# Kernel optimization log

Measured on AMD Instinct MI355X. Metric: run time of the kernel, lower is better.

## Reference

```python
import jax, jax.numpy as jnp
import numpy as np

B, M, N, K = 8192, 512, 2048, 16
P = 50      # top-k support size per iteration
EPS = 0.01


def soft_threshold(x, theta, p):
    # x: [B, N]
    if p == 0:
        return jnp.sign(x) * jax.nn.relu(jnp.abs(x) - theta)
    abs_ = jnp.abs(x)
    topk_vals, _ = jax.lax.top_k(abs_, p)          # sorted descending
    thresh = topk_vals[:, -1]                      # min of top-k, per row
    keep = (abs_ > thresh[:, None]).astype(x.dtype)
    shrunk = jnp.sign(x) * jax.nn.relu(abs_ - theta)
    return keep * x + (1.0 - keep) * shrunk


def setup_inputs() -> dict:
    key = jax.random.key(0)
    k_y, k_A = jax.random.split(key)
    y = jax.random.normal(k_y, (B, M), dtype=jnp.float32)
    A = jax.random.normal(k_A, (M, N), dtype=jnp.float32) / np.sqrt(M)
    gamma = jnp.full((K,), 3.0, dtype=jnp.float32)
    theta = jnp.full((K,), 0.02, dtype=jnp.float32)
    a_param = jnp.full((K,), 0.01, dtype=jnp.float32)
    v = jnp.ones((K,), dtype=jnp.float32)
    vu = jnp.full((K,), 0.05, dtype=jnp.float32)
    theta_init = jnp.float32(1.0)
    return {"y": y, "A": A, "gamma": gamma, "theta": theta,
            "a_param": a_param, "v": v, "vu": vu,
            "theta_init": theta_init, "info": 0}


def reference(y, A, gamma, theta, a_param, v, vu, theta_init, info):
    # forward_op(x)  = x @ A.T   : [B,N] -> [B,M]
    # backward_op(b) = b @ A     : [B,M] -> [B,N]
    x = jnp.zeros((y.shape[0], A.shape[1]), dtype=y.dtype)
    for i in range(K):
        t = theta_init if i == 0 else theta[i]
        gain = 1.0 + t * vu[i] * jnp.exp(-v[i] * jnp.abs(x))
        b = (gain * x) @ A.T - y                 # residual in measurement space
        c = b @ A                                # gradient step direction
        x_new = soft_threshold(x - gamma[i] * c, theta[i], P)
        overshoot = 1.0 + a_param[i] / (jnp.abs(x_new - x) + EPS)
        x = overshoot * x_new + (1.0 - overshoot) * x
    return (x, jnp.zeros((K, 1), dtype=y.dtype), jnp.zeros((K, 1), dtype=y.dtype))
```

## Files before the change

### kernel.cpp

```cpp
#include <hip/hip_runtime.h>
#include <math.h>

#define Bsz  8192
#define Mdim 512
#define Ndim 2048
#define Kit  16
#define Pk   50
#define EPSv 0.01f

typedef __attribute__((ext_vector_type(8))) short bf16x8;
typedef __attribute__((ext_vector_type(4))) float f32x4;

static __device__ __forceinline__ unsigned short f2bf(float f) {
    unsigned u = __float_as_uint(f);
    return (unsigned short)((u + 0x7fffu + ((u >> 16) & 1u)) >> 16);
}
static __device__ __forceinline__ float bf2f(unsigned short h) {
    return __uint_as_float(((unsigned)h) << 16);
}

static __device__ __forceinline__ void gl16(const void* g, void* l) {
    __builtin_amdgcn_global_load_lds(
        (const __attribute__((address_space(1))) unsigned int*)g,
        (__attribute__((address_space(3))) unsigned int*)l, 16, 0, 0);
}

#define PIPE_BARRIER() __builtin_amdgcn_s_barrier()

#define MFMA3(acc_, bh_, bl_, ah_, al_)                                         \
    acc_ = __builtin_amdgcn_mfma_f32_16x16x32_bf16(bh_, ah_, acc_, 0, 0, 0);    \
    acc_ = __builtin_amdgcn_mfma_f32_16x16x32_bf16(bh_, al_, acc_, 0, 0, 0);    \
    acc_ = __builtin_amdgcn_mfma_f32_16x16x32_bf16(bl_, ah_, acc_, 0, 0, 0);

__global__ __launch_bounds__(256) void presplit_A(
    const float* __restrict__ A, unsigned short* __restrict__ Ah,
    unsigned short* __restrict__ Al, unsigned short* __restrict__ AhT,
    unsigned short* __restrict__ AlT)
{
    int idx = blockIdx.x * 256 + threadIdx.x;
    int m = idx >> 11, n = idx & (Ndim - 1);
    float a = A[idx];
    unsigned short h = f2bf(a);
    unsigned short l = f2bf(a - bf2f(h));
    Ah[idx] = h; Al[idx] = l;
    AhT[(size_t)n * Mdim + m] = h;
    AlT[(size_t)n * Mdim + m] = l;
}

__global__ __launch_bounds__(256) void split_negy_kernel(const float* __restrict__ y,
                                                         unsigned short* __restrict__ bS) {
    int i = blockIdx.x * 256 + threadIdx.x;
    float4 v = ((const float4*)y)[i];
    int idx = i * 4;
    int r = idx >> 9, c = idx & 511;
    float f0 = -v.x, f1 = -v.y, f2 = -v.z, f3 = -v.w;
    unsigned short h0 = f2bf(f0), h1 = f2bf(f1), h2 = f2bf(f2), h3 = f2bf(f3);
    ushort4 hv = make_ushort4(h0, h1, h2, h3);
    ushort4 lv = make_ushort4(f2bf(f0 - bf2f(h0)), f2bf(f1 - bf2f(h1)),
                              f2bf(f2 - bf2f(h2)), f2bf(f3 - bf2f(h3)));
    *(ushort4*)(bS + (size_t)r * 1024 + c)       = hv;
    *(ushort4*)(bS + (size_t)r * 1024 + 512 + c) = lv;
}

__global__ __launch_bounds__(256) void gemm1_mfma(
    const unsigned short* __restrict__ zS,
    const unsigned short* __restrict__ Ah, const unsigned short* __restrict__ Al,
    const float* __restrict__ y, unsigned short* __restrict__ bS)
{
    const int tid  = threadIdx.x;
    const int lane = tid & 63, w = tid >> 6;
    const int lm   = lane & 15, quad = lane >> 4;
    const int wr   = (w & 1) * 64, wm = (w >> 1) * 32;

    int d   = blockIdx.y * gridDim.x + blockIdx.x;
    int sid = (d & 7) * 64 + (d >> 3);
    const int m0 = (sid & 7) * 64, r0 = (sid >> 3) * 128;

    __shared__ __attribute__((aligned(16))) unsigned short zh_s[128 * 64];
    __shared__ __attribute__((aligned(16))) unsigned short zl_s[128 * 64];
    __shared__ __attribute__((aligned(16))) unsigned short ah_s[64 * 64];
    __shared__ __attribute__((aligned(16))) unsigned short al_s[64 * 64];

    f32x4 acc[4][2];
#pragma unroll
    for (int i = 0; i < 4; i++)
#pragma unroll
        for (int j = 0; j < 2; j++) acc[i][j] = (f32x4)0.f;

    const unsigned short* zsh[4]; const unsigned short* zsl[4]; int zoff[4];
#pragma unroll
    for (int s = 0; s < 4; s++) {
        int off = ((w * 4 + s) << 10) + lane * 16;
        int row = off >> 7;
        int kb  = (off & 127) ^ ((row & 7) << 4);
        zoff[s] = (w * 4 + s) << 10;
        zsh[s]  = zS + (size_t)(r0 + row) * 4096 + (kb >> 1);
        zsl[s]  = zS + (size_t)(r0 + row) * 4096 + 2048 + (kb >> 1);
    }
    const unsigned short* ash[2]; const unsigned short* asl[2]; int aoff[2];
#pragma unroll
    for (int s = 0; s < 2; s++) {
        int off = ((w * 2 + s) << 10) + lane * 16;
        int row = off >> 7;
        int kb  = (off & 127) ^ ((row & 7) << 4);
        aoff[s] = (w * 2 + s) << 10;
        ash[s]  = Ah + (size_t)(m0 + row) * 2048 + (kb >> 1);
        asl[s]  = Al + (size_t)(m0 + row) * 2048 + (kb >> 1);
    }

    const int X = (lm & 7) << 4;

    for (int k0 = 0; k0 < Ndim; k0 += 64) {
        __syncthreads();
#pragma unroll
        for (int s = 0; s < 4; s++) {
            gl16(zsh[s], (char*)zh_s + zoff[s]);
            gl16(zsl[s], (char*)zl_s + zoff[s]);
            zsh[s] += 64; zsl[s] += 64;
        }
#pragma unroll
        for (int s = 0; s < 2; s++) {
            gl16(ash[s], (char*)ah_s + aoff[s]);
            gl16(asl[s], (char*)al_s + aoff[s]);
            ash[s] += 64; asl[s] += 64;
        }
        __syncthreads();
#pragma unroll
        for (int kk = 0; kk < 2; kk++) {
            const int cbx = (kk * 64 + quad * 16) ^ X;
            bf16x8 bhf[2], blf[2];
#pragma unroll
            for (int fj = 0; fj < 2; fj++) {
                int ar = wm + fj * 16 + lm;
                bhf[fj] = *(const bf16x8*)((const char*)ah_s + ar * 128 + cbx);
                blf[fj] = *(const bf16x8*)((const char*)al_s + ar * 128 + cbx);
            }
#pragma unroll
            for (int fi = 0; fi < 4; fi++) {
                int zr = wr + fi * 16 + lm;
                bf16x8 zh8 = *(const bf16x8*)((const char*)zh_s + zr * 128 + cbx);
                bf16x8 zl8 = *(const bf16x8*)((const char*)zl_s + zr * 128 + cbx);
#pragma unroll
                for (int fj = 0; fj < 2; fj++) {
                    MFMA3(acc[fi][fj], zh8, zl8, bhf[fj], blf[fj]);
                }
            }
        }
    }
#pragma unroll
    for (int fi = 0; fi < 4; fi++)
#pragma unroll
        for (int fj = 0; fj < 2; fj++)
#pragma unroll
            for (int r = 0; r < 4; r++) {
                int row = r0 + wr + fi * 16 + quad * 4 + r;
                int col = m0 + wm + fj * 16 + lm;
                float bv = acc[fi][fj][r] - y[(size_t)row * Mdim + col];
                unsigned short h = f2bf(bv);
                bS[(size_t)row * 1024 + col]       = h;
                bS[(size_t)row * 1024 + 512 + col] = f2bf(bv - bf2f(h));
            }
}

__global__ __launch_bounds__(512, 2) void gemm2_mfma(
    const unsigned short* __restrict__ bS,
    const unsigned short* __restrict__ AhT, const unsigned short* __restrict__ AlT,
    float* __restrict__ c)
{
    enum { NT = 16 };
    const int tid  = threadIdx.x;
    const int lane = tid & 63, w = tid >> 6;
    const int lm   = lane & 15, quad = lane >> 4;
    const int wrow = (w >> 2) * 128;
    const int wcol = (w & 3) * 64;

    int d   = blockIdx.y * gridDim.x + blockIdx.x;
    int sid = (d & 7) * 32 + (d >> 3);
    const int n0 = (sid & 7) * 256, r0 = (sid >> 3) * 256;

    __shared__ __attribute__((aligned(16))) unsigned short smem[2 * 32768];

    f32x4 acc[8][4];
#pragma unroll
    for (int i = 0; i < 8; i++)
#pragma unroll
        for (int j = 0; j < 4; j++) acc[i][j] = (f32x4)0.f;

    const unsigned short *bhp[2], *blp[2], *ahp[2], *alp[2]; int doff[2];
#pragma unroll
    for (int s = 0; s < 2; s++) {
        int off = ((w * 2 + s) << 10) + lane * 16;
        int row = off >> 6;
        int kb  = (off & 63) ^ (((row >> 1) & 3) << 4);
        doff[s] = (w * 2 + s) << 10;
        bhp[s]  = bS  + (size_t)(r0 + row) * 1024 + (kb >> 1);
        blp[s]  = bS  + (size_t)(r0 + row) * 1024 + 512 + (kb >> 1);
        ahp[s]  = AhT + (size_t)(n0 + row) * 512 + (kb >> 1);
        alp[s]  = AlT + (size_t)(n0 + row) * 512 + (kb >> 1);
    }

    const int X   = ((lm >> 1) & 3) << 4;
    const int cbx = (quad * 16) ^ X;

    auto STAGE = [&](int t) {
        char* base = (char*)smem + (t & 1) * 65536;
        const int ko = t * 32;
#pragma unroll
        for (int s = 0; s < 2; s++) {
            gl16(bhp[s] + ko, base +     0 + doff[s]);
            gl16(blp[s] + ko, base + 16384 + doff[s]);
            gl16(ahp[s] + ko, base + 32768 + doff[s]);
            gl16(alp[s] + ko, base + 49152 + doff[s]);
        }
    };

    STAGE(0);
    asm volatile("s_waitcnt vmcnt(0)" ::: "memory");
    PIPE_BARRIER();

#pragma unroll 2
    for (int t = 0; t < NT; ++t) {
        const char* B0  = (const char*)smem + (t & 1) * 65536;
        const char* bhB = B0, *blB = B0 + 16384;
        const char* ahB = B0 + 32768, *alB = B0 + 49152;

        bf16x8 ahf[4], alf[4], bhf[4], blf[4];
#pragma unroll
        for (int fj = 0; fj < 4; fj++) {
            int ar = wcol + fj * 16 + lm;
            ahf[fj] = *(const bf16x8*)(ahB + ar * 64 + cbx);
            alf[fj] = *(const bf16x8*)(alB + ar * 64 + cbx);
        }
#pragma unroll
        for (int fi = 0; fi < 4; fi++) {
            int br = wrow + fi * 16 + lm;
            bhf[fi] = *(const bf16x8*)(bhB + br * 64 + cbx);
            blf[fi] = *(const bf16x8*)(blB + br * 64 + cbx);
        }
        if (t + 1 < NT) STAGE(t + 1);
        PIPE_BARRIER();
        asm volatile("s_waitcnt lgkmcnt(0)" ::: "memory");
        __builtin_amdgcn_sched_barrier(0);
        __builtin_amdgcn_s_setprio(1);
#pragma unroll
        for (int fi = 0; fi < 4; fi++)
#pragma unroll
            for (int fj = 0; fj < 4; fj++) {
                MFMA3(acc[fi][fj], bhf[fi], blf[fi], ahf[fj], alf[fj]);
            }
        __builtin_amdgcn_s_setprio(0);
        PIPE_BARRIER();

#pragma unroll
        for (int fi = 0; fi < 4; fi++) {
            int br = wrow + (fi + 4) * 16 + lm;
            bhf[fi] = *(const bf16x8*)(bhB + br * 64 + cbx);
            blf[fi] = *(const bf16x8*)(blB + br * 64 + cbx);
        }
        PIPE_BARRIER();
        asm volatile("s_waitcnt lgkmcnt(0)" ::: "memory");
        __builtin_amdgcn_sched_barrier(0);
        __builtin_amdgcn_s_setprio(1);
#pragma unroll
        for (int fi = 0; fi < 4; fi++)
#pragma unroll
            for (int fj = 0; fj < 4; fj++) {
                MFMA3(acc[fi + 4][fj], bhf[fi], blf[fi], ahf[fj], alf[fj]);
            }
        __builtin_amdgcn_s_setprio(0);
        asm volatile("s_waitcnt vmcnt(0)" ::: "memory");
        PIPE_BARRIER();
    }

#pragma unroll
    for (int fi = 0; fi < 8; fi++)
#pragma unroll
        for (int fj = 0; fj < 4; fj++)
#pragma unroll
            for (int r = 0; r < 4; r++) {
                int row = r0 + wrow + fi * 16 + quad * 4 + r;
                int col = n0 + wcol + fj * 16 + lm;
                c[(size_t)row * Ndim + col] = acc[fi][fj][r];
            }
}

__global__ __launch_bounds__(256) void topk_update_kernel(
    float* __restrict__ uz, float* __restrict__ x,
    const float* __restrict__ gamma, const float* __restrict__ theta,
    const float* __restrict__ a_param, const float* __restrict__ vv,
    const float* __restrict__ vu, int it)
{
    const int row = blockIdx.x;
    const int t   = threadIdx.x;
    float* crow = uz + (size_t)row * Ndim;
    float* xrow = x  + (size_t)row * Ndim;
    const float g = gamma[it];

    float4 c0 = *(const float4*)(crow + 4 * t);
    float4 c1 = *(const float4*)(crow + 4 * t + 1024);
    float4 x0 = *(const float4*)(xrow + 4 * t);
    float4 x1 = *(const float4*)(xrow + 4 * t + 1024);
    float cv[8] = { c0.x, c0.y, c0.z, c0.w, c1.x, c1.y, c1.z, c1.w };
    float xv[8] = { x0.x, x0.y, x0.z, x0.w, x1.x, x1.y, x1.z, x1.w };

    float uvals[8];
    unsigned keys[8];
#pragma unroll
    for (int e = 0; e < 8; e++) {
        uvals[e] = xv[e] - g * cv[e];
        keys[e]  = __float_as_uint(fabsf(uvals[e]));
    }

    __shared__ unsigned bins[256];
    __shared__ unsigned sel[2];

    unsigned prefix = 0;
    unsigned k = Pk;
#pragma unroll
    for (int pass = 0; pass < 4; ++pass) {
        const int shift = 24 - pass * 8;
        bins[t] = 0;
        __syncthreads();
        const unsigned himask = (pass == 0) ? 0u : (0xFFFFFFFFu << (shift + 8));
#pragma unroll
        for (int e = 0; e < 8; e++) {
            if ((keys[e] & himask) == prefix)
                atomicAdd(&bins[(keys[e] >> shift) & 255], 1u);
        }
        __syncthreads();
        if (t < 64) {
            const int i0 = 255 - 4 * t;
            unsigned c0b = bins[i0], c1b = bins[i0 - 1];
            unsigned c2b = bins[i0 - 2], c3b = bins[i0 - 3];
            unsigned s = c0b + c1b + c2b + c3b;
            unsigned sc = s;
#pragma unroll
            for (int off = 1; off < 64; off <<= 1) {
                unsigned o = __shfl_up(sc, (unsigned)off);
                if (t >= off) sc += o;
            }
            unsigned pre = sc - s;
            unsigned cs[4] = { c0b, c1b, c2b, c3b };
#pragma unroll
            for (int j = 0; j < 4; j++) {
                unsigned cb = cs[j];
                if (pre < k && pre + cb >= k) { sel[0] = (unsigned)(i0 - j); sel[1] = k - pre; }
                pre += cb;
            }
        }
        __syncthreads();
        prefix |= sel[0] << shift;
        k = sel[1];
    }
    const float thresh = __uint_as_float(prefix);

    const float th = theta[it];
    const float ap = a_param[it];
    const bool haveNext = (it + 1) < Kit;
    float tn = 0.f, vn = 0.f, vun = 0.f;
    if (haveNext) { tn = theta[it + 1]; vn = vv[it + 1]; vun = vu[it + 1]; }

    float xo[8];
    unsigned short zh8[8], zl8[8];
#pragma unroll
    for (int e = 0; e < 8; e++) {
        float uval = uvals[e];
        float au   = fabsf(uval);
        bool keep  = au > thresh;
        float shr  = copysignf(fmaxf(au - th, 0.f), uval);
        float xn   = keep ? uval : shr;
        float dlt  = xn - xv[e];
        float ov   = 1.f + ap / (fabsf(dlt) + EPSv);
        float xr   = xv[e] + ov * dlt;
        xo[e] = xr;
        float z = (1.f + tn * vun * __expf(-vn * fabsf(xr))) * xr;
        unsigned short h = f2bf(z);
        zh8[e] = h;
        zl8[e] = f2bf(z - bf2f(h));
    }
    float4 a0 = { xo[0], xo[1], xo[2], xo[3] };
    float4 a1 = { xo[4], xo[5], xo[6], xo[7] };
    *(float4*)(xrow + 4 * t) = a0;
    *(float4*)(xrow + 4 * t + 1024) = a1;
    if (haveNext) {
        unsigned short* zp = (unsigned short*)crow;
        *(ushort4*)(zp + 4 * t)        = make_ushort4(zh8[0], zh8[1], zh8[2], zh8[3]);
        *(ushort4*)(zp + 1024 + 4 * t) = make_ushort4(zh8[4], zh8[5], zh8[6], zh8[7]);
        *(ushort4*)(zp + 2048 + 4 * t) = make_ushort4(zl8[0], zl8[1], zl8[2], zl8[3]);
        *(ushort4*)(zp + 3072 + 4 * t) = make_ushort4(zl8[4], zl8[5], zl8[6], zl8[7]);
    }
}

extern "C" void kernel_launch(void* const* d_in, const int* in_sizes, int n_in,
                              void* d_out, int out_size, void* d_ws, size_t ws_size,
                              hipStream_t stream) {
    const float* y       = (const float*)d_in[0];
    const float* A       = (const float*)d_in[1];
    const float* gamma   = (const float*)d_in[2];
    const float* theta   = (const float*)d_in[3];
    const float* a_param = (const float*)d_in[4];
    const float* v       = (const float*)d_in[5];
    const float* vu      = (const float*)d_in[6];

    float* x = (float*)d_out;

    char* ws = (char*)d_ws;
    float*          uz = (float*)ws;
    unsigned short* bS = (unsigned short*)(ws + (size_t)Bsz * Ndim * 4);
    unsigned short* Ah = (unsigned short*)(ws + (size_t)80 * 1024 * 1024);
    unsigned short* Al  = Ah  + (size_t)Mdim * Ndim;
    unsigned short* AhT = Al  + (size_t)Mdim * Ndim;
    unsigned short* AlT = AhT + (size_t)Mdim * Ndim;

    hipMemsetAsync(d_out, 0, (size_t)out_size * sizeof(float), stream);

    dim3 g1(Mdim / 64, Bsz / 128);
    dim3 g2(Ndim / 256, Bsz / 256);

    presplit_A<<<(Mdim * Ndim) / 256, dim3(256), 0, stream>>>(A, Ah, Al, AhT, AlT);
    split_negy_kernel<<<(Bsz * Mdim / 4) / 256, dim3(256), 0, stream>>>(y, bS);

    for (int it = 0; it < Kit; ++it) {
        if (it > 0)
            gemm1_mfma<<<g1, dim3(256), 0, stream>>>((const unsigned short*)uz, Ah, Al, y, bS);
        gemm2_mfma<<<g2, dim3(512), 0, stream>>>(bS, AhT, AlT, uz);
        topk_update_kernel<<<Bsz, dim3(256), 0, stream>>>(uz, x, gamma, theta, a_param, v, vu, it);
    }
}
```

Before: 2.566 ms.

## Double-buffer gemm1 with split-K wave groups, larger tiles, and radix-11 top-k

```diff
diff --git a/kernel.cpp b/kernel.cpp
--- a/kernel.cpp
+++ b/kernel.cpp
@@ -62,104 +62,150 @@
     *(ushort4*)(bS + (size_t)r * 1024 + 512 + c) = lv;
 }
 
-__global__ __launch_bounds__(256) void gemm1_mfma(
+__global__ __launch_bounds__(512, 2) void gemm1_mfma(
     const unsigned short* __restrict__ zS,
     const unsigned short* __restrict__ Ah, const unsigned short* __restrict__ Al,
     const float* __restrict__ y, unsigned short* __restrict__ bS)
 {
+    enum { NT = 32 };
     const int tid  = threadIdx.x;
     const int lane = tid & 63, w = tid >> 6;
     const int lm   = lane & 15, quad = lane >> 4;
-    const int wr   = (w & 1) * 64, wm = (w >> 1) * 32;
+    const int g    = w >> 2;
+    const int wg   = w & 3;
+    const int wrow = (wg >> 1) * 64;
+    const int wcol = (wg & 1) * 64;
 
     int d   = blockIdx.y * gridDim.x + blockIdx.x;
-    int sid = (d & 7) * 64 + (d >> 3);
-    const int m0 = (sid & 7) * 64, r0 = (sid >> 3) * 128;
-
-    __shared__ __attribute__((aligned(16))) unsigned short zh_s[128 * 64];
-    __shared__ __attribute__((aligned(16))) unsigned short zl_s[128 * 64];
-    __shared__ __attribute__((aligned(16))) unsigned short ah_s[64 * 64];
-    __shared__ __attribute__((aligned(16))) unsigned short al_s[64 * 64];
-
-    f32x4 acc[4][2];
+    int sid = (d & 7) * 32 + (d >> 3);
+    const int m0 = (sid & 3) * 128, r0 = (sid >> 2) * 128;
+
+    __shared__ __attribute__((aligned(16))) unsigned short smem[2 * 32768];
+
+    f32x4 acc[4][4];
 #pragma unroll
     for (int i = 0; i < 4; i++)
 #pragma unroll
-        for (int j = 0; j < 2; j++) acc[i][j] = (f32x4)0.f;
-
-    const unsigned short* zsh[4]; const unsigned short* zsl[4]; int zoff[4];
-#pragma unroll
-    for (int s = 0; s < 4; s++) {
-        int off = ((w * 4 + s) << 10) + lane * 16;
-        int row = off >> 7;
-        int kb  = (off & 127) ^ ((row & 7) << 4);
-        zoff[s] = (w * 4 + s) << 10;
-        zsh[s]  = zS + (size_t)(r0 + row) * 4096 + (kb >> 1);
-        zsl[s]  = zS + (size_t)(r0 + row) * 4096 + 2048 + (kb >> 1);
-    }
-    const unsigned short* ash[2]; const unsigned short* asl[2]; int aoff[2];
+        for (int j = 0; j < 4; j++) acc[i][j] = (f32x4)0.f;
+
+    const unsigned short *zhp[2], *zlp[2], *ahp[2], *alp[2]; int doff[2];
 #pragma unroll
     for (int s = 0; s < 2; s++) {
-        int off = ((w * 2 + s) << 10) + lane * 16;
-        int row = off >> 7;
-        int kb  = (off & 127) ^ ((row & 7) << 4);
-        aoff[s] = (w * 2 + s) << 10;
-        ash[s]  = Ah + (size_t)(m0 + row) * 2048 + (kb >> 1);
-        asl[s]  = Al + (size_t)(m0 + row) * 2048 + (kb >> 1);
-    }
-
-    const int X = (lm & 7) << 4;
-
-    for (int k0 = 0; k0 < Ndim; k0 += 64) {
-        __syncthreads();
-#pragma unroll
-        for (int s = 0; s < 4; s++) {
-            gl16(zsh[s], (char*)zh_s + zoff[s]);
-            gl16(zsl[s], (char*)zl_s + zoff[s]);
-            zsh[s] += 64; zsl[s] += 64;
-        }
+        int off = ((wg * 2 + s) << 10) + lane * 16;
+        int row = off >> 6;
+        int kb  = (off & 63) ^ (((row >> 1) & 3) << 4);
+        doff[s] = (wg * 2 + s) << 10;
+        int kbase = g * 1024 + (kb >> 1);
+        zhp[s]  = zS + (size_t)(r0 + row) * 4096 + kbase;
+        zlp[s]  = zS + (size_t)(r0 + row) * 4096 + 2048 + kbase;
+        ahp[s]  = Ah + (size_t)(m0 + row) * 2048 + kbase;
+        alp[s]  = Al + (size_t)(m0 + row) * 2048 + kbase;
+    }
+
+    const int X   = ((lm >> 1) & 3) << 4;
+    const int cbx = (quad * 16) ^ X;
+
+    auto STAGE = [&](int t) {
+        char* base = (char*)smem + (t & 1) * 65536 + g * 32768;
+        const int ko = t * 32;
 #pragma unroll
         for (int s = 0; s < 2; s++) {
-            gl16(ash[s], (char*)ah_s + aoff[s]);
-            gl16(asl[s], (char*)al_s + aoff[s]);
-            ash[s] += 64; asl[s] += 64;
-        }
-        __syncthreads();
-#pragma unroll
-        for (int kk = 0; kk < 2; kk++) {
-            const int cbx = (kk * 64 + quad * 16) ^ X;
-            bf16x8 bhf[2], blf[2];
-#pragma unroll
-            for (int fj = 0; fj < 2; fj++) {
-                int ar = wm + fj * 16 + lm;
-                bhf[fj] = *(const bf16x8*)((const char*)ah_s + ar * 128 + cbx);
-                blf[fj] = *(const bf16x8*)((const char*)al_s + ar * 128 + cbx);
-            }
-#pragma unroll
-            for (int fi = 0; fi < 4; fi++) {
-                int zr = wr + fi * 16 + lm;
-                bf16x8 zh8 = *(const bf16x8*)((const char*)zh_s + zr * 128 + cbx);
-                bf16x8 zl8 = *(const bf16x8*)((const char*)zl_s + zr * 128 + cbx);
-#pragma unroll
-                for (int fj = 0; fj < 2; fj++) {
-                    MFMA3(acc[fi][fj], zh8, zl8, bhf[fj], blf[fj]);
+            gl16(zhp[s] + ko, base +     0 + doff[s]);
+            gl16(zlp[s] + ko, base +  8192 + doff[s]);
+            gl16(ahp[s] + ko, base + 16384 + doff[s]);
+            gl16(alp[s] + ko, base + 24576 + doff[s]);
+        }
+    };
+
+    STAGE(0);
+    asm volatile("s_waitcnt vmcnt(0)" ::: "memory");
+    PIPE_BARRIER();
+
+#pragma unroll 2
+    for (int t = 0; t < NT; ++t) {
+        const char* B0  = (const char*)smem + (t & 1) * 65536 + g * 32768;
+        const char* zhB = B0, *zlB = B0 + 8192;
+        const char* ahB = B0 + 16384, *alB = B0 + 24576;
+
+        bf16x8 ahf[4], alf[4], zhf[2], zlf[2];
+#pragma unroll
+        for (int fj = 0; fj < 4; fj++) {
+            int ar = wcol + fj * 16 + lm;
+            ahf[fj] = *(const bf16x8*)(ahB + ar * 64 + cbx);
+            alf[fj] = *(const bf16x8*)(alB + ar * 64 + cbx);
+        }
+#pragma unroll
+        for (int fi = 0; fi < 2; fi++) {
+            int zr = wrow + fi * 16 + lm;
+            zhf[fi] = *(const bf16x8*)(zhB + zr * 64 + cbx);
+            zlf[fi] = *(const bf16x8*)(zlB + zr * 64 + cbx);
+        }
+        if (t + 1 < NT) STAGE(t + 1);
+        PIPE_BARRIER();
+        asm volatile("s_waitcnt lgkmcnt(0)" ::: "memory");
+        __builtin_amdgcn_sched_barrier(0);
+        __builtin_amdgcn_s_setprio(1);
+#pragma unroll
+        for (int fi = 0; fi < 2; fi++)
+#pragma unroll
+            for (int fj = 0; fj < 4; fj++) {
+                MFMA3(acc[fi][fj], zhf[fi], zlf[fi], ahf[fj], alf[fj]);
+            }
+        __builtin_amdgcn_s_setprio(0);
+        PIPE_BARRIER();
+
+#pragma unroll
+        for (int fi = 0; fi < 2; fi++) {
+            int zr = wrow + (fi + 2) * 16 + lm;
+            zhf[fi] = *(const bf16x8*)(zhB + zr * 64 + cbx);
+            zlf[fi] = *(const bf16x8*)(zlB + zr * 64 + cbx);
+        }
+        PIPE_BARRIER();
+        asm volatile("s_waitcnt lgkmcnt(0)" ::: "memory");
+        __builtin_amdgcn_sched_barrier(0);
+        __builtin_amdgcn_s_setprio(1);
+#pragma unroll
+        for (int fi = 0; fi < 2; fi++)
+#pragma unroll
+            for (int fj = 0; fj < 4; fj++) {
+                MFMA3(acc[fi + 2][fj], zhf[fi], zlf[fi], ahf[fj], alf[fj]);
+            }
+        __builtin_amdgcn_s_setprio(0);
+        asm volatile("s_waitcnt vmcnt(0)" ::: "memory");
+        PIPE_BARRIER();
+    }
+
+    float* cmb = (float*)smem;
+    __syncthreads();
+    if (g == 1) {
+#pragma unroll
+        for (int fi = 0; fi < 4; fi++)
+#pragma unroll
+            for (int fj = 0; fj < 4; fj++)
+#pragma unroll
+                for (int r = 0; r < 4; r++) {
+                    int row = wrow + fi * 16 + quad * 4 + r;
+                    int col = wcol + fj * 16 + lm;
+                    cmb[row * 132 + col] = acc[fi][fj][r];
                 }
-            }
-        }
-    }
-#pragma unroll
-    for (int fi = 0; fi < 4; fi++)
-#pragma unroll
-        for (int fj = 0; fj < 2; fj++)
-#pragma unroll
-            for (int r = 0; r < 4; r++) {
-                int row = r0 + wr + fi * 16 + quad * 4 + r;
-                int col = m0 + wm + fj * 16 + lm;
-                float bv = acc[fi][fj][r] - y[(size_t)row * Mdim + col];
-                unsigned short h = f2bf(bv);
-                bS[(size_t)row * 1024 + col]       = h;
-                bS[(size_t)row * 1024 + 512 + col] = f2bf(bv - bf2f(h));
-            }
+    }
+    __syncthreads();
+    if (g == 0) {
+#pragma unroll
+        for (int fi = 0; fi < 4; fi++)
+#pragma unroll
+            for (int fj = 0; fj < 4; fj++)
+#pragma unroll
+                for (int r = 0; r < 4; r++) {
+                    int row = wrow + fi * 16 + quad * 4 + r;
+                    int col = wcol + fj * 16 + lm;
+                    float bv = acc[fi][fj][r] + cmb[row * 132 + col]
+                             - y[(size_t)(r0 + row) * Mdim + (m0 + col)];
+                    unsigned short h = f2bf(bv);
+                    bS[(size_t)(r0 + row) * 1024 + (m0 + col)]       = h;
+                    bS[(size_t)(r0 + row) * 1024 + 512 + (m0 + col)] = f2bf(bv - bf2f(h));
+                }
+    }
 }
 
 __global__ __launch_bounds__(512, 2) void gemm2_mfma(
@@ -311,41 +357,55 @@
         keys[e]  = __float_as_uint(fabsf(uvals[e]));
     }
 
-    __shared__ unsigned bins[256];
+    __shared__ unsigned bins[2048];
     __shared__ unsigned sel[2];
+    __shared__ unsigned wsum[4];
 
     unsigned prefix = 0;
     unsigned k = Pk;
 #pragma unroll
-    for (int pass = 0; pass < 4; ++pass) {
-        const int shift = 24 - pass * 8;
-        bins[t] = 0;
+    for (int pass = 0; pass < 3; ++pass) {
+        const int      shift  = (pass == 0) ? 20 : (pass == 1) ? 9 : 0;
+        const unsigned cmask  = (pass == 2) ? 511u : 2047u;
+        const unsigned himask = (pass == 0) ? 0u
+                              : (pass == 1) ? (0xFFFFFFFFu << 20)
+                                            : (0xFFFFFFFFu << 9);
+        uint4 zz = { 0u, 0u, 0u, 0u };
+        ((uint4*)bins)[t]       = zz;
+        ((uint4*)bins)[t + 256] = zz;
         __syncthreads();
-        const unsigned himask = (pass == 0) ? 0u : (0xFFFFFFFFu << (shift + 8));
 #pragma unroll
         for (int e = 0; e < 8; e++) {
             if ((keys[e] & himask) == prefix)
-                atomicAdd(&bins[(keys[e] >> shift) & 255], 1u);
+                atomicAdd(&bins[(keys[e] >> shift) & cmask], 1u);
         }
         __syncthreads();
-        if (t < 64) {
-            const int i0 = 255 - 4 * t;
-            unsigned c0b = bins[i0], c1b = bins[i0 - 1];
-            unsigned c2b = bins[i0 - 2], c3b = bins[i0 - 3];
-            unsigned s = c0b + c1b + c2b + c3b;
-            unsigned sc = s;
-#pragma unroll
-            for (int off = 1; off < 64; off <<= 1) {
-                unsigned o = __shfl_up(sc, (unsigned)off);
-                if (t >= off) sc += o;
-            }
-            unsigned pre = sc - s;
-            unsigned cs[4] = { c0b, c1b, c2b, c3b };
-#pragma unroll
-            for (int j = 0; j < 4; j++) {
-                unsigned cb = cs[j];
-                if (pre < k && pre + cb >= k) { sel[0] = (unsigned)(i0 - j); sel[1] = k - pre; }
-                pre += cb;
+        const int base = 2040 - 8 * t;
+        uint4 q0 = *(const uint4*)&bins[base];
+        uint4 q1 = *(const uint4*)&bins[base + 4];
+        unsigned s  = q0.x + q0.y + q0.z + q0.w + q1.x + q1.y + q1.z + q1.w;
+        unsigned sc = s;
+        const int ln = t & 63;
+#pragma unroll
+        for (int off = 1; off < 64; off <<= 1) {
+            unsigned o = __shfl_up(sc, (unsigned)off);
+            if (ln >= off) sc += o;
+        }
+        if (ln == 63) wsum[t >> 6] = sc;
+        __syncthreads();
+        unsigned wpre = 0;
+#pragma unroll
+        for (int ww = 0; ww < 3; ww++)
+            if (ww < (t >> 6)) wpre += wsum[ww];
+        unsigned pre = wpre + sc - s;
+        if (pre < k && pre + s >= k) {
+            unsigned vals[8] = { q1.w, q1.z, q1.y, q1.x, q0.w, q0.z, q0.y, q0.x };
+            unsigned p2 = pre;
+#pragma unroll
+            for (int j = 0; j < 8; j++) {
+                unsigned cb = vals[j];
+                if (p2 < k && p2 + cb >= k) { sel[0] = (unsigned)(base + 7 - j); sel[1] = k - p2; }
+                p2 += cb;
             }
         }
         __syncthreads();
@@ -414,7 +474,7 @@
 
     hipMemsetAsync(d_out, 0, (size_t)out_size * sizeof(float), stream);
 
-    dim3 g1(Mdim / 64, Bsz / 128);
+    dim3 g1(Mdim / 128, Bsz / 128);
     dim3 g2(Ndim / 256, Bsz / 256);
 
     presplit_A<<<(Mdim * Ndim) / 256, dim3(256), 0, stream>>>(A, Ah, Al, AhT, AlT);
@@ -422,7 +482,7 @@
 
     for (int it = 0; it < Kit; ++it) {
         if (it > 0)
-            gemm1_mfma<<<g1, dim3(256), 0, stream>>>((const unsigned short*)uz, Ah, Al, y, bS);
+            gemm1_mfma<<<g1, dim3(512), 0, stream>>>((const unsigned short*)uz, Ah, Al, y, bS);
         gemm2_mfma<<<g2, dim3(512), 0, stream>>>(bS, AhT, AlT, uz);
         topk_update_kernel<<<Bsz, dim3(256), 0, stream>>>(uz, x, gamma, theta, a_param, v, vu, it);
     }
```

After: 2.424 ms. -5.6%, faster.
